# Kernel tuning notes

Hardware: AMD Instinct MI355X
Metric: run time of the kernel (lower is better)

The kernel has to match this reference:

```python
import jax, jax.numpy as jnp
import numpy as np

ALPHA = 0.2  # LeakyReLU negative slope


def _gat_layer(h, dst, adj, w, a_in, a_out, b):
    # h: [N, F_in], dst: [N, K] int (edge (i,k): i -> dst[i,k]), adj: [N, K]
    hid = h @ w                      # [N, D]
    s_in = hid @ a_in                # [N]  (attention applied to source-node half)
    s_out = hid @ a_out              # [N]  (attention applied to dest-node half)
    # edge scores, grouped per source node (matches view(-1, num_neighs) softmax)
    e = jax.nn.leaky_relu(s_in[:, None] + s_out[dst], ALPHA)   # [N, K]
    # torch code detaches attention (Variable(..., requires_grad=False))
    att = jax.lax.stop_gradient(jax.nn.softmax(e, axis=1))     # [N, K]
    w_edge = adj * att                                          # [N, K]
    # SpMM: out[i] = sum_k w_edge[i,k] * hid[dst[i,k]]
    out = jnp.einsum('nk,nkd->nd', w_edge, hid[dst]) + b        # [N, D]
    return out


def setup_inputs() -> dict:
    key = jax.random.key(0)
    ks = jax.random.split(key, 12)
    N, K, F, H, O = 100000, 16, 128, 128, 128
    stdv1 = 1.0 / np.sqrt(H)
    stdv2 = 1.0 / np.sqrt(O)
    u = lambda k, shp, s: jax.random.uniform(k, shp, jnp.float32, -s, s)
    return {
        'x': jax.random.normal(ks[0], (N, F), jnp.float32),
        'dst_idx': jax.random.randint(ks[1], (N, K), 0, N),
        'adj_vals': jax.random.uniform(ks[2], (N, K), jnp.float32),
        'w1': u(ks[3], (F, H), stdv1),
        'a_in1': jax.random.normal(ks[4], (H,), jnp.float32) * (1.414 / np.sqrt(H)),
        'a_out1': jax.random.normal(ks[5], (H,), jnp.float32) * (1.414 / np.sqrt(H)),
        'b1': u(ks[6], (H,), stdv1),
        'w2': u(ks[7], (H, O), stdv2),
        'a_in2': jax.random.normal(ks[8], (O,), jnp.float32) * (1.414 / np.sqrt(O)),
        'a_out2': jax.random.normal(ks[9], (O,), jnp.float32) * (1.414 / np.sqrt(O)),
        'b2': u(ks[10], (O,), stdv2),
    }


def reference(x, dst_idx, adj_vals, w1, a_in1, a_out1, b1, w2, a_in2, a_out2, b2):
    h = jax.nn.relu(_gat_layer(x, dst_idx, adj_vals, w1, a_in1, a_out1, b1))
    h = jax.nn.relu(_gat_layer(h, dst_idx, adj_vals, w2, a_in2, a_out2, b2))
    return h
```

## Files before the change

kernel.cpp:

```cpp
#include <hip/hip_runtime.h>

#define ALPHA 0.2f
#define LDA 136

typedef short bf16x8 __attribute__((ext_vector_type(8)));
typedef float f32x4  __attribute__((ext_vector_type(4)));

static __device__ __forceinline__ float bf2f(unsigned short u) {
    union { unsigned int i; float f; } v; v.i = ((unsigned int)u) << 16; return v.f;
}
static __device__ __forceinline__ unsigned short f2bf(float f) {
    union { float f; unsigned int i; } v; v.f = f;
    unsigned int x = v.i;
    return (unsigned short)((x + 0x7fffu + ((x >> 16) & 1u)) >> 16);
}

__global__ __launch_bounds__(128)
void prep_wT_kernel(const float* __restrict__ w1, const float* __restrict__ w2,
                    unsigned short* __restrict__ wT1, unsigned short* __restrict__ wT2)
{
    const int b = blockIdx.x;
    const float* w = (b >> 4) ? w2 : w1;
    unsigned short* wT = (b >> 4) ? wT2 : wT1;
    const int k0 = (b & 15) * 8;
    const int c = threadIdx.x;

    ushort4 u0, u1;
    u0.x = f2bf(w[(k0 + 0) * 128 + c]); u0.y = f2bf(w[(k0 + 1) * 128 + c]);
    u0.z = f2bf(w[(k0 + 2) * 128 + c]); u0.w = f2bf(w[(k0 + 3) * 128 + c]);
    u1.x = f2bf(w[(k0 + 4) * 128 + c]); u1.y = f2bf(w[(k0 + 5) * 128 + c]);
    u1.z = f2bf(w[(k0 + 6) * 128 + c]); u1.w = f2bf(w[(k0 + 7) * 128 + c]);
    *(ushort4*)&wT[c * 128 + k0]     = u0;
    *(ushort4*)&wT[c * 128 + k0 + 4] = u1;
}

template <bool SRC_BF>
__global__ __launch_bounds__(256, 4)
void gemm_score_mfma(const void* __restrict__ srcv,
                     const unsigned short* __restrict__ wT,
                     const float* __restrict__ a_in,
                     const float* __restrict__ a_out,
                     unsigned short* __restrict__ hid,
                     float* __restrict__ s_in,
                     float* __restrict__ s_out,
                     int n)
{
    __shared__ short Bs[128 * LDA];
    __shared__ float aS[2][128];

    const int tid  = threadIdx.x;
    const int lane = tid & 63;
    const int wv   = tid >> 6;
    const int m    = lane & 15;
    const int q    = lane >> 4;
    const int rbase = blockIdx.x * 64;
    const int row   = rbase + wv * 16 + m;
    const bool rok  = (row < n);

    if (tid < 128) { aS[0][tid] = a_in[tid]; aS[1][tid] = a_out[tid]; }

    bf16x8 aF[4];
    if (SRC_BF) {
        const unsigned short* src = (const unsigned short*)srcv;
        const unsigned short* p = &src[(size_t)row * 128 + q * 8];
        #pragma unroll
        for (int ks = 0; ks < 4; ks++)
            aF[ks] = rok ? *(const bf16x8*)(p + ks * 32) : (bf16x8){0,0,0,0,0,0,0,0};
    } else {
        const float* src = (const float*)srcv;
        const float* p = &src[(size_t)row * 128 + q * 8];
        #pragma unroll
        for (int ks = 0; ks < 4; ks++) {
            if (rok) {
                float4 v0 = *(const float4*)(p + ks * 32);
                float4 v1 = *(const float4*)(p + ks * 32 + 4);
                bf16x8 a;
                a[0] = (short)f2bf(v0.x); a[1] = (short)f2bf(v0.y);
                a[2] = (short)f2bf(v0.z); a[3] = (short)f2bf(v0.w);
                a[4] = (short)f2bf(v1.x); a[5] = (short)f2bf(v1.y);
                a[6] = (short)f2bf(v1.z); a[7] = (short)f2bf(v1.w);
                aF[ks] = a;
            } else aF[ks] = (bf16x8){0,0,0,0,0,0,0,0};
        }
    }

    #pragma unroll
    for (int i = 0; i < 8; i++) {
        int e = tid + i * 256;
        int nr = e >> 4, j = (e & 15) * 8;
        int4 v = *(const int4*)&wT[nr * 128 + j];
        *(int4*)&Bs[nr * LDA + j] = v;
    }
    __syncthreads();

    f32x4 acc[8];
    #pragma unroll
    for (int t = 0; t < 8; t++) acc[t] = (f32x4){0.f, 0.f, 0.f, 0.f};

    const short* Bbase = &Bs[m * LDA + q * 8];
    #pragma unroll
    for (int ks = 0; ks < 4; ks++) {
        #pragma unroll
        for (int t = 0; t < 8; t++) {
            bf16x8 bF = *(const bf16x8*)(Bbase + t * 16 * LDA + ks * 32);
            acc[t] = __builtin_amdgcn_mfma_f32_16x16x32_bf16(aF[ks], bF, acc[t], 0, 0, 0);
        }
    }

    float pin[4] = {0.f, 0.f, 0.f, 0.f}, pout[4] = {0.f, 0.f, 0.f, 0.f};
    #pragma unroll
    for (int t = 0; t < 8; t++) {
        float ai = aS[0][t * 16 + m];
        float ao = aS[1][t * 16 + m];
        #pragma unroll
        for (int r = 0; r < 4; r++) {
            pin[r]  += acc[t][r] * ai;
            pout[r] += acc[t][r] * ao;
        }
    }
    #pragma unroll
    for (int msk = 8; msk >= 1; msk >>= 1) {
        #pragma unroll
        for (int r = 0; r < 4; r++) {
            pin[r]  += __shfl_xor(pin[r],  msk);
            pout[r] += __shfl_xor(pout[r], msk);
        }
    }
    if (m == 0) {
        #pragma unroll
        for (int r = 0; r < 4; r++) {
            int g = rbase + wv * 16 + q * 4 + r;
            if (g < n) { s_in[g] = pin[r]; s_out[g] = pout[r]; }
        }
    }

    __syncthreads();
    short* Es = Bs;
    #pragma unroll
    for (int t = 0; t < 8; t++)
        #pragma unroll
        for (int r = 0; r < 4; r++)
            Es[(wv * 16 + q * 4 + r) * LDA + t * 16 + m] = (short)f2bf(acc[t][r]);
    __syncthreads();
    #pragma unroll
    for (int i = 0; i < 4; i++) {
        int e = tid + i * 256;
        int r = e >> 4, j = (e & 15) * 8;
        int gr = rbase + r;
        if (gr < n) {
            int4 v = *(const int4*)&Es[r * LDA + j];
            *(int4*)&hid[(size_t)gr * 128 + j] = v;
        }
    }
}

template <bool FINAL>
__global__ __launch_bounds__(256)
void gat_aggregate_kernel(const unsigned short* __restrict__ hid,
                          const float* __restrict__ s_in,
                          const float* __restrict__ s_out,
                          const int* __restrict__ dst,
                          const float* __restrict__ adj,
                          const float* __restrict__ bias,
                          void* __restrict__ outv,
                          int n)
{
    const int lane = threadIdx.x & 63;
    const int node = (blockIdx.x * 256 + threadIdx.x) >> 6;
    if (node >= n) return;

    float sc = -1e30f;
    int dk = 0;
    float av = 0.f;
    if (lane < 16) {
        int ei = node * 16 + lane;
        dk = dst[ei];
        av = adj[ei];
        float e = s_in[node] + s_out[dk];
        sc = (e > 0.f) ? e : ALPHA * e;
    }
    float m = sc;
    #pragma unroll
    for (int msk = 8; msk >= 1; msk >>= 1) m = fmaxf(m, __shfl_xor(m, msk));
    float p = (lane < 16) ? __expf(sc - m) : 0.f;
    float s = p;
    #pragma unroll
    for (int msk = 8; msk >= 1; msk >>= 1) s += __shfl_xor(s, msk);
    float wk = (lane < 16) ? av * p / s : 0.f;

    const int c = lane * 2;
    float accx = 0.f, accy = 0.f;
    #pragma unroll
    for (int k = 0; k < 16; k++) {
        int   sdk = __builtin_amdgcn_readlane(dk, k);
        float swk = __int_as_float(__builtin_amdgcn_readlane(__float_as_int(wk), k));
        ushort2 hq = *(const ushort2*)&hid[(size_t)sdk * 128 + c];
        accx += swk * bf2f(hq.x);
        accy += swk * bf2f(hq.y);
    }
    float ox = fmaxf(accx + bias[c],     0.f);
    float oy = fmaxf(accy + bias[c + 1], 0.f);

    const size_t oidx = (size_t)node * 128 + c;
    if (FINAL) {
        *(float2*)&((float*)outv)[oidx] = make_float2(ox, oy);
    } else {
        ushort2 ov; ov.x = f2bf(ox); ov.y = f2bf(oy);
        *(ushort2*)&((unsigned short*)outv)[oidx] = ov;
    }
}

extern "C" void kernel_launch(void* const* d_in, const int* in_sizes, int n_in,
                              void* d_out, int out_size, void* d_ws, size_t ws_size,
                              hipStream_t stream)
{
    const float* x      = (const float*)d_in[0];
    const int*   dst    = (const int*)d_in[1];
    const float* adj    = (const float*)d_in[2];
    const float* w1     = (const float*)d_in[3];
    const float* a_in1  = (const float*)d_in[4];
    const float* a_out1 = (const float*)d_in[5];
    const float* b1     = (const float*)d_in[6];
    const float* w2     = (const float*)d_in[7];
    const float* a_in2  = (const float*)d_in[8];
    const float* a_out2 = (const float*)d_in[9];
    const float* b2     = (const float*)d_in[10];

    const int N = in_sizes[0] / 128;

    unsigned short* hid   = (unsigned short*)d_ws;
    float*          s_in  = (float*)(hid + (size_t)N * 128);
    float*          s_out = s_in + N;
    unsigned short* wT1   = (unsigned short*)(s_out + N);
    unsigned short* wT2   = wT1 + 128 * 128;
    unsigned short* h1    = (unsigned short*)d_out + out_size;

    dim3 blk(256);
    dim3 ggrid((N + 63) / 64);
    dim3 agrid((N + 3) / 4);

    prep_wT_kernel<<<32, 128, 0, stream>>>(w1, w2, wT1, wT2);

    gemm_score_mfma<false><<<ggrid, blk, 0, stream>>>(x,  wT1, a_in1, a_out1,
                                                      hid, s_in, s_out, N);
    gat_aggregate_kernel<false><<<agrid, blk, 0, stream>>>(hid, s_in, s_out, dst,
                                                           adj, b1, h1, N);
    gemm_score_mfma<true><<<ggrid, blk, 0, stream>>>(h1, wT2, a_in2, a_out2,
                                                     hid, s_in, s_out, N);
    gat_aggregate_kernel<true><<<agrid, blk, 0, stream>>>(hid, s_in, s_out, dst,
                                                          adj, b2, d_out, N);
}
```

Measured before the change: 259.3 us.

## Fuse layer-1 aggregation with layer-2 GEMM and score computation

Layer-1 neighbour aggregation and the layer-2 projection GEMM with attention scores now run in one kernel. Each block aggregates 64 nodes into a shared-memory tile, then applies the MFMA GEMM directly to that tile. This removes the global write and re-read of the intermediate h1 activations and one kernel launch. In exchange it adds a larger shared-memory footprint that may reduce occupancy, plus a serial 16-node loop per wave during the gather phase. Separate score buffers are kept for each layer so that layer 2's scores do not overwrite layer 1's while they are still being read.

Result: no change. 256.7 us (-1.0%).

```diff
diff --git a/kernel.cpp b/kernel.cpp
--- a/kernel.cpp
+++ b/kernel.cpp
@@ -34,9 +34,8 @@
     *(ushort4*)&wT[c * 128 + k0 + 4] = u1;
 }
 
-template <bool SRC_BF>
 __global__ __launch_bounds__(256, 4)
-void gemm_score_mfma(const void* __restrict__ srcv,
+void gemm_score_mfma(const float* __restrict__ src,
                      const unsigned short* __restrict__ wT,
                      const float* __restrict__ a_in,
                      const float* __restrict__ a_out,
@@ -60,14 +59,7 @@
     if (tid < 128) { aS[0][tid] = a_in[tid]; aS[1][tid] = a_out[tid]; }
 
     bf16x8 aF[4];
-    if (SRC_BF) {
-        const unsigned short* src = (const unsigned short*)srcv;
-        const unsigned short* p = &src[(size_t)row * 128 + q * 8];
-        #pragma unroll
-        for (int ks = 0; ks < 4; ks++)
-            aF[ks] = rok ? *(const bf16x8*)(p + ks * 32) : (bf16x8){0,0,0,0,0,0,0,0};
-    } else {
-        const float* src = (const float*)srcv;
+    {
         const float* p = &src[(size_t)row * 128 + q * 8];
         #pragma unroll
         for (int ks = 0; ks < 4; ks++) {
@@ -154,16 +146,173 @@
     }
 }
 
-template <bool FINAL>
 __global__ __launch_bounds__(256)
-void gat_aggregate_kernel(const unsigned short* __restrict__ hid,
-                          const float* __restrict__ s_in,
-                          const float* __restrict__ s_out,
-                          const int* __restrict__ dst,
-                          const float* __restrict__ adj,
-                          const float* __restrict__ bias,
-                          void* __restrict__ outv,
-                          int n)
+void fused_agg_gemm(const unsigned short* __restrict__ hid1,
+                    const float* __restrict__ s_in1,
+                    const float* __restrict__ s_out1,
+                    const int* __restrict__ dst,
+                    const float* __restrict__ adj,
+                    const float* __restrict__ bias1,
+                    const unsigned short* __restrict__ wT2,
+                    const float* __restrict__ a_in2,
+                    const float* __restrict__ a_out2,
+                    unsigned short* __restrict__ hid2,
+                    float* __restrict__ s_in2,
+                    float* __restrict__ s_out2,
+                    int n)
+{
+    __shared__ short As[64 * LDA];
+    __shared__ short Bs[128 * LDA];
+    __shared__ float aS[2][128];
+
+    const int tid  = threadIdx.x;
+    const int lane = tid & 63;
+    const int wv   = tid >> 6;
+    const int rbase = blockIdx.x * 64;
+
+    if (tid < 128) { aS[0][tid] = a_in2[tid]; aS[1][tid] = a_out2[tid]; }
+
+    #pragma unroll
+    for (int i = 0; i < 8; i++) {
+        int e = tid + i * 256;
+        int nr = e >> 4, j = (e & 15) * 8;
+        int4 v = *(const int4*)&wT2[nr * 128 + j];
+        *(int4*)&Bs[nr * LDA + j] = v;
+    }
+
+    const int jn  = lane >> 2;
+    const int kq  = lane & 3;
+    const int node = rbase + wv * 16 + jn;
+    const bool nok = (node < n);
+
+    int4   dk4 = make_int4(0, 0, 0, 0);
+    float4 av4 = make_float4(0.f, 0.f, 0.f, 0.f);
+    float  si  = 0.f;
+    if (nok) {
+        dk4 = *(const int4*)&dst[node * 16 + kq * 4];
+        av4 = *(const float4*)&adj[node * 16 + kq * 4];
+        si  = s_in1[node];
+    }
+    float e0 = si + s_out1[dk4.x], e1 = si + s_out1[dk4.y];
+    float e2 = si + s_out1[dk4.z], e3 = si + s_out1[dk4.w];
+    e0 = (e0 > 0.f) ? e0 : ALPHA * e0;  e1 = (e1 > 0.f) ? e1 : ALPHA * e1;
+    e2 = (e2 > 0.f) ? e2 : ALPHA * e2;  e3 = (e3 > 0.f) ? e3 : ALPHA * e3;
+    float mx = fmaxf(fmaxf(e0, e1), fmaxf(e2, e3));
+    mx = fmaxf(mx, __shfl_xor(mx, 1));
+    mx = fmaxf(mx, __shfl_xor(mx, 2));
+    float p0 = __expf(e0 - mx), p1 = __expf(e1 - mx);
+    float p2 = __expf(e2 - mx), p3 = __expf(e3 - mx);
+    float sm = p0 + p1 + p2 + p3;
+    sm += __shfl_xor(sm, 1);
+    sm += __shfl_xor(sm, 2);
+    const float inv = __frcp_rn(sm);
+    float4 wk4 = make_float4(av4.x * p0 * inv, av4.y * p1 * inv,
+                             av4.z * p2 * inv, av4.w * p3 * inv);
+
+    const int c = lane * 2;
+    const float2 bia = *(const float2*)&bias1[c];
+
+    for (int j2 = 0; j2 < 16; j2++) {
+        float accx = 0.f, accy = 0.f;
+        #pragma unroll
+        for (int k = 0; k < 16; k++) {
+            const int srcl = j2 * 4 + (k >> 2);
+            int   sdk, swki;
+            if ((k & 3) == 0) { sdk = __builtin_amdgcn_readlane(dk4.x, srcl);
+                                swki = __builtin_amdgcn_readlane(__float_as_int(wk4.x), srcl); }
+            else if ((k & 3) == 1) { sdk = __builtin_amdgcn_readlane(dk4.y, srcl);
+                                swki = __builtin_amdgcn_readlane(__float_as_int(wk4.y), srcl); }
+            else if ((k & 3) == 2) { sdk = __builtin_amdgcn_readlane(dk4.z, srcl);
+                                swki = __builtin_amdgcn_readlane(__float_as_int(wk4.z), srcl); }
+            else             { sdk = __builtin_amdgcn_readlane(dk4.w, srcl);
+                                swki = __builtin_amdgcn_readlane(__float_as_int(wk4.w), srcl); }
+            float swk = __int_as_float(swki);
+            ushort2 hq = *(const ushort2*)&hid1[(size_t)sdk * 128 + c];
+            accx += swk * bf2f(hq.x);
+            accy += swk * bf2f(hq.y);
+        }
+        float ox = fmaxf(accx + bia.x, 0.f);
+        float oy = fmaxf(accy + bia.y, 0.f);
+        ushort2 hv; hv.x = f2bf(ox); hv.y = f2bf(oy);
+        *(ushort2*)&As[(wv * 16 + j2) * LDA + c] = hv;
+    }
+    __syncthreads();
+
+    const int m = lane & 15;
+    const int q = lane >> 4;
+
+    f32x4 acc[8];
+    #pragma unroll
+    for (int t = 0; t < 8; t++) acc[t] = (f32x4){0.f, 0.f, 0.f, 0.f};
+
+    const short* Abase = &As[(wv * 16 + m) * LDA + q * 8];
+    const short* Bbase = &Bs[m * LDA + q * 8];
+    #pragma unroll
+    for (int ks = 0; ks < 4; ks++) {
+        bf16x8 aF = *(const bf16x8*)(Abase + ks * 32);
+        #pragma unroll
+        for (int t = 0; t < 8; t++) {
+            bf16x8 bF = *(const bf16x8*)(Bbase + t * 16 * LDA + ks * 32);
+            acc[t] = __builtin_amdgcn_mfma_f32_16x16x32_bf16(aF, bF, acc[t], 0, 0, 0);
+        }
+    }
+
+    float pin[4] = {0.f, 0.f, 0.f, 0.f}, pout[4] = {0.f, 0.f, 0.f, 0.f};
+    #pragma unroll
+    for (int t = 0; t < 8; t++) {
+        float ai = aS[0][t * 16 + m];
+        float ao = aS[1][t * 16 + m];
+        #pragma unroll
+        for (int r = 0; r < 4; r++) {
+            pin[r]  += acc[t][r] * ai;
+            pout[r] += acc[t][r] * ao;
+        }
+    }
+    #pragma unroll
+    for (int msk = 8; msk >= 1; msk >>= 1) {
+        #pragma unroll
+        for (int r = 0; r < 4; r++) {
+            pin[r]  += __shfl_xor(pin[r],  msk);
+            pout[r] += __shfl_xor(pout[r], msk);
+        }
+    }
+    if (m == 0) {
+        #pragma unroll
+        for (int r = 0; r < 4; r++) {
+            int g = rbase + wv * 16 + q * 4 + r;
+            if (g < n) { s_in2[g] = pin[r]; s_out2[g] = pout[r]; }
+        }
+    }
+
+    __syncthreads();
+    short* Es = As;
+    #pragma unroll
+    for (int t = 0; t < 8; t++)
+        #pragma unroll
+        for (int r = 0; r < 4; r++)
+            Es[(wv * 16 + q * 4 + r) * LDA + t * 16 + m] = (short)f2bf(acc[t][r]);
+    __syncthreads();
+    #pragma unroll
+    for (int i = 0; i < 4; i++) {
+        int e = tid + i * 256;
+        int r = e >> 4, j = (e & 15) * 8;
+        int gr = rbase + r;
+        if (gr < n) {
+            int4 v = *(const int4*)&Es[r * LDA + j];
+            *(int4*)&hid2[(size_t)gr * 128 + j] = v;
+        }
+    }
+}
+
+__global__ __launch_bounds__(256)
+void gat_aggregate_final(const unsigned short* __restrict__ hid,
+                         const float* __restrict__ s_in,
+                         const float* __restrict__ s_out,
+                         const int* __restrict__ dst,
+                         const float* __restrict__ adj,
+                         const float* __restrict__ bias,
+                         float* __restrict__ out,
+                         int n)
 {
     const int lane = threadIdx.x & 63;
     const int node = (blockIdx.x * 256 + threadIdx.x) >> 6;
@@ -200,14 +349,7 @@
     }
     float ox = fmaxf(accx + bias[c],     0.f);
     float oy = fmaxf(accy + bias[c + 1], 0.f);
-
-    const size_t oidx = (size_t)node * 128 + c;
-    if (FINAL) {
-        *(float2*)&((float*)outv)[oidx] = make_float2(ox, oy);
-    } else {
-        ushort2 ov; ov.x = f2bf(ox); ov.y = f2bf(oy);
-        *(ushort2*)&((unsigned short*)outv)[oidx] = ov;
-    }
+    *(float2*)&out[(size_t)node * 128 + c] = make_float2(ox, oy);
 }
 
 extern "C" void kernel_launch(void* const* d_in, const int* in_sizes, int n_in,
@@ -228,12 +370,14 @@
 
     const int N = in_sizes[0] / 128;
 
-    unsigned short* hid   = (unsigned short*)d_ws;
-    float*          s_in  = (float*)(hid + (size_t)N * 128);
-    float*          s_out = s_in + N;
-    unsigned short* wT1   = (unsigned short*)(s_out + N);
+    unsigned short* hid2  = (unsigned short*)d_ws;
+    float*          s_in1 = (float*)(hid2 + (size_t)N * 128);
+    float*          s_out1= s_in1 + N;
+    float*          s_in2 = s_out1 + N;
+    float*          s_out2= s_in2 + N;
+    unsigned short* wT1   = (unsigned short*)(s_out2 + N);
     unsigned short* wT2   = wT1 + 128 * 128;
-    unsigned short* h1    = (unsigned short*)d_out + out_size;
+    unsigned short* hid1  = (unsigned short*)d_out + out_size;
 
     dim3 blk(256);
     dim3 ggrid((N + 63) / 64);
@@ -241,12 +385,11 @@
 
     prep_wT_kernel<<<32, 128, 0, stream>>>(w1, w2, wT1, wT2);
 
-    gemm_score_mfma<false><<<ggrid, blk, 0, stream>>>(x,  wT1, a_in1, a_out1,
-                                                      hid, s_in, s_out, N);
-    gat_aggregate_kernel<false><<<agrid, blk, 0, stream>>>(hid, s_in, s_out, dst,
-                                                           adj, b1, h1, N);
-    gemm_score_mfma<true><<<ggrid, blk, 0, stream>>>(h1, wT2, a_in2, a_out2,
-                                                     hid, s_in, s_out, N);
-    gat_aggregate_kernel<true><<<agrid, blk, 0, stream>>>(hid, s_in, s_out, dst,
-                                                          adj, b2, d_out, N);
-}
+    gemm_score_mfma<<<ggrid, blk, 0, stream>>>(x, wT1, a_in1, a_out1,
+                                               hid1, s_in1, s_out1, N);
+    fused_agg_gemm<<<ggrid, blk, 0, stream>>>(hid1, s_in1, s_out1, dst, adj, b1,
+                                              wT2, a_in2, a_out2,
+                                              hid2, s_in2, s_out2, N);
+    gat_aggregate_final<<<agrid, blk, 0, stream>>>(hid2, s_in2, s_out2, dst, adj,
+                                                   b2, (float*)d_out, N);
+}
```
